# Optimization experiments

Hardware: AMD Instinct MI355X
Metric: run time of the kernel (lower is better)

## Reference

```python
import jax, jax.numpy as jnp
import numpy as np
import math

N_NODES, N_EDGES, NNZ, D, L = 100000, 20000, 500000, 128, 4
ALPHA, LAMDA = 0.1, 0.5


def setup_inputs() -> dict:
    key = jax.random.key(0)
    ks = jax.random.split(key, 16)
    x = jax.random.normal(ks[0], (N_NODES, D), jnp.float32)
    e = jax.random.normal(ks[1], (N_EDGES, D), jnp.float32)
    nodes = jax.random.randint(ks[2], (NNZ,), 0, N_NODES)
    edges = jnp.sort(jax.random.randint(ks[3], (NNZ,), 0, N_EDGES)).at[-1].set(N_EDGES - 1)
    hyperedge_index = jnp.stack([nodes, edges]).astype(jnp.int32)
    dist_v2e = jax.random.randint(ks[4], (NNZ,), 0, 64).astype(jnp.float32)
    deg_v2e = jax.random.randint(ks[5], (NNZ,), 0, 64).astype(jnp.float32)
    dist_e2v = jax.random.randint(ks[6], (NNZ,), 0, 64).astype(jnp.float32)
    deg_e2v = jax.random.randint(ks[7], (NNZ,), 0, 64).astype(jnp.float32)
    s = 0.05
    W0 = jax.random.normal(ks[8], (D, D), jnp.float32) * s
    b0 = jnp.zeros((D,), jnp.float32)
    Wn = jax.random.normal(ks[9], (L, D, D), jnp.float32) * s
    We = jax.random.normal(ks[10], (L, D, D), jnp.float32) * s
    attn_w = jax.random.normal(ks[11], (L, 2 * D), jnp.float32) * s
    attn_b = jnp.zeros((L,), jnp.float32)
    wd_w = jax.random.normal(ks[12], (L,), jnp.float32) * s
    wd_b = jnp.zeros((L,), jnp.float32)
    wg_w = jax.random.normal(ks[13], (L,), jnp.float32) * s
    wg_b = jnp.zeros((L,), jnp.float32)
    return dict(x=x, e=e, hyperedge_index=hyperedge_index, dist_v2e=dist_v2e,
                deg_v2e=deg_v2e, dist_e2v=dist_e2v, deg_e2v=deg_e2v,
                W0=W0, b0=b0, Wn=Wn, We=We, attn_w=attn_w, attn_b=attn_b,
                wd_w=wd_w, wd_b=wd_b, wg_w=wg_w, wg_b=wg_b)


def _seg_softmax(s, idx, num):
    # numerically-stable scatter_softmax over segments idx
    m = jax.ops.segment_max(s, idx, num_segments=num)
    ex = jnp.exp(s - m[idx])
    den = jax.ops.segment_sum(ex, idx, num_segments=num)
    return ex / den[idx]


def _forward(x, e, hei, dv2e, gv2e, de2v, ge2v, W0, b0, Wn, We, aw, ab, wdw, wdb, wgw, wgb):
    nodes, edges = hei[0], hei[1]
    N, E = x.shape[0], e.shape[0]
    ones = jnp.ones(nodes.shape[0], x.dtype)
    dV = jax.ops.segment_sum(ones, nodes, num_segments=N)
    cnt = jax.ops.segment_sum(ones, edges, num_segments=E)
    dE = jax.ops.segment_sum(dV[nodes], edges, num_segments=E) / jnp.maximum(cnt, 1.0)
    degV = jnp.where(dV > 0, dV ** -0.5, 1.0)[:, None]   # [N,1]
    degE = jnp.where(dE > 0, dE ** -0.5, 1.0)[:, None]   # [E,1]

    x = jax.nn.relu(x @ W0 + b0)
    x0, e0 = x, e
    d = x.shape[1]
    for i in range(L):
        beta = math.log(LAMDA / (i + 1) + 1.0)
        # v2e attention: concat [x[nodes], e[edges]] -> softmax over edge segments
        sx1 = x @ aw[i, :d]; se1 = e @ aw[i, d:]
        s_v2e = sx1[nodes] + se1[edges] + ab[i] + dv2e * wdw[i] + wdb[i] + gv2e * wgw[i] + wgb[i]
        a_v2e = _seg_softmax(s_v2e, edges, E)[:, None]
        # e2v attention (flipped): concat [e[edges], x[nodes]] -> softmax over node segments
        se2 = e @ aw[i, :d]; sx2 = x @ aw[i, d:]
        s_e2v = se2[edges] + sx2[nodes] + ab[i] + de2v * wdw[i] + wdb[i] + ge2v * wgw[i] + wgb[i]
        a_e2v = _seg_softmax(s_e2v, nodes, N)[:, None]

        Xe1 = jax.ops.segment_sum(x[nodes] * a_v2e, edges, num_segments=E) * degE
        Xv1 = jax.ops.segment_sum(Xe1[edges] * a_e2v, nodes, num_segments=N) * degV
        Xv2 = jax.ops.segment_sum(e[edges] * a_e2v, nodes, num_segments=N) * degV
        Xe2 = jax.ops.segment_sum(Xv2[nodes] * a_v2e, edges, num_segments=E) * degE
        xm = (Xv1 + Xv2) * 0.5
        em = (Xe1 + Xe2) * 0.5
        xi = (1 - ALPHA) * xm + ALPHA * x0
        x = (1 - beta) * xi + beta * (xi @ Wn[i])
        ei = (1 - ALPHA) * em + ALPHA * e0
        e = (1 - beta) * ei + beta * (ei @ We[i])
        if i < L - 1:
            x = jax.nn.relu(x)
            e = jax.nn.relu(e)
    return x, e


def reference(x, e, hyperedge_index, dist_v2e, deg_v2e, dist_e2v, deg_e2v,
              W0, b0, Wn, We, attn_w, attn_b, wd_w, wd_b, wg_w, wg_b):
    return _forward(x, e, hyperedge_index, dist_v2e, deg_v2e, dist_e2v, deg_e2v,
                    W0, b0, Wn, We, attn_w, attn_b, wd_w, wd_b, wg_w, wg_b)
```

## Files before the change

### kernel.cpp

```cpp
#include <hip/hip_runtime.h>
#include <hip/hip_fp16.h>
#include <math.h>

#define DD 128
#define SCAN_BLOCKS 256
#define SMAX_CAP 128

typedef _Float16 f16x8 __attribute__((ext_vector_type(8)));
typedef float f32x4 __attribute__((ext_vector_type(4)));

__device__ inline float wave_sum(float v){
#pragma unroll
  for (int m = 32; m >= 1; m >>= 1) v += __shfl_xor(v, m, 64);
  return v;
}
__device__ inline int wave_sum_i(int v){
#pragma unroll
  for (int m = 32; m >= 1; m >>= 1) v += __shfl_xor(v, m, 64);
  return v;
}


__global__ void k_edge_offsets(const int* __restrict__ edges, int nnz, int E,
                               int* __restrict__ eo){
  int e = blockIdx.x * blockDim.x + threadIdx.x;
  if (e > E) return;
  int lo = 0, hi = nnz;
  while (lo < hi){ int mid = (lo + hi) >> 1; if (edges[mid] < e) lo = mid + 1; else hi = mid; }
  eo[e] = lo;
}

__global__ void k_hist(const int* __restrict__ nodes, int nnz, int* __restrict__ dV){
  int k = blockIdx.x * blockDim.x + threadIdx.x;
  if (k < nnz) atomicAdd(&dV[nodes[k]], 1);
}

__global__ __launch_bounds__(256) void k_scan_partial(const int* __restrict__ dV, int N,
                                                      int* __restrict__ part){
  int b = blockIdx.x, t = threadIdx.x;
  int chunk = (N + SCAN_BLOCKS - 1) / SCAN_BLOCKS;
  int s0 = b * chunk, s1 = min(s0 + chunk, N);
  int sum = 0;
  for (int n = s0 + t; n < s1; n += 256) sum += dV[n];
  sum = wave_sum_i(sum);
  __shared__ int wred[4];
  int lane = t & 63, wid = t >> 6;
  if (lane == 0) wred[wid] = sum;
  __syncthreads();
  if (t == 0) part[b] = wred[0] + wred[1] + wred[2] + wred[3];
}

__global__ __launch_bounds__(SCAN_BLOCKS) void k_scan_blocksums(int* __restrict__ part){
  __shared__ int sh[SCAN_BLOCKS];
  int t = threadIdx.x;
  int v = part[t];
  sh[t] = v; __syncthreads();
  for (int off = 1; off < SCAN_BLOCKS; off <<= 1){
    int add = (t >= off) ? sh[t - off] : 0;
    __syncthreads();
    sh[t] += add;
    __syncthreads();
  }
  part[t] = sh[t] - v;
}

__global__ __launch_bounds__(256) void k_scan_apply(const int* __restrict__ dV, int N, int nnz,
    const int* __restrict__ partScan, int* __restrict__ no, int* __restrict__ nfill,
    float* __restrict__ degV){
  int b = blockIdx.x, t = threadIdx.x;
  int chunk = (N + SCAN_BLOCKS - 1) / SCAN_BLOCKS;
  int s0 = b * chunk, s1 = min(s0 + chunk, N);
  int lane = t & 63, wid = t >> 6;
  __shared__ int wtot[4];
  __shared__ int s_run;
  if (t == 0) s_run = partScan[b];
  __syncthreads();
  for (int base = s0; base < s1; base += 256){
    int n = base + t;
    int d = (n < s1) ? dV[n] : 0;
    int v = d;
#pragma unroll
    for (int off = 1; off < 64; off <<= 1){
      int o = __shfl_up(v, off, 64);
      if (lane >= off) v += o;
    }
    if (lane == 63) wtot[wid] = v;
    __syncthreads();
    int run0 = s_run;
    int woff = 0;
    for (int w = 0; w < wid; w++) woff += wtot[w];
    if (n < s1){
      int excl = run0 + woff + v - d;
      no[n] = excl; nfill[n] = excl;
      degV[n] = d > 0 ? 1.0f / sqrtf((float)d) : 1.0f;
    }
    int btot = wtot[0] + wtot[1] + wtot[2] + wtot[3];
    __syncthreads();
    if (t == 0) s_run = run0 + btot;
    __syncthreads();
  }
  if (b == 0 && t == 0) no[N] = nnz;
}

__global__ void k_permpack(const int* __restrict__ nodes, const int* __restrict__ edges,
                           const float* __restrict__ dist, const float* __restrict__ deg,
                           int nnz, int* __restrict__ nfill, float2* __restrict__ pack){
  int k = blockIdx.x * blockDim.x + threadIdx.x;
  if (k < nnz){
    int pos = atomicAdd(&nfill[nodes[k]], 1);
    pack[pos] = make_float2(__int_as_float(edges[k]), dist[k] + 64.f * deg[k]);
  }
}

__global__ void k_edge_deg(const int* __restrict__ nodes, const int* __restrict__ eo, int E,
                           const int* __restrict__ dV, float* __restrict__ degE){
  int e = blockIdx.x * blockDim.x + threadIdx.x;
  if (e >= E) return;
  int b = eo[e], en = eo[e + 1];
  float s = 0.f;
  for (int k = b; k < en; k++) s += (float)dV[nodes[k]];
  float cnt = (float)(en - b);
  float dE = s / fmaxf(cnt, 1.0f);
  degE[e] = dE > 0.f ? 1.0f / sqrtf(dE) : 1.0f;
}

__global__ __launch_bounds__(256) void k_einit(const float2* __restrict__ e_in2,
    const float* __restrict__ aw1, const float* __restrict__ aw2,
    int E, __half2* __restrict__ e0h,
    float* __restrict__ se1, float* __restrict__ se2){
  int wave = threadIdx.x >> 6, lane = threadIdx.x & 63;
  int e = blockIdx.x * 4 + wave;
  if (e >= E) return;
  float2 v = e_in2[(size_t)e * 64 + lane];
  e0h[(size_t)e * 64 + lane] = __floats2half2_rn(v.x, v.y);
  float2 a2v = ((const float2*)aw2)[lane];
  float2 a1v = ((const float2*)aw1)[lane];
  float s1 = v.x * a2v.x + v.y * a2v.y;
  float s2 = v.x * a1v.x + v.y * a1v.y;
  s1 = wave_sum(s1); s2 = wave_sum(s2);
  if (lane == 0){ se1[e] = s1; se2[e] = s2; }
}

__global__ void k_wcast(const float* __restrict__ W0, const float* __restrict__ Wn,
                        const float* __restrict__ We, _Float16* __restrict__ Wt){
  int idx = blockIdx.x * 256 + threadIdx.x;
  if (idx >= 9 * 16384) return;
  int m = idx >> 14, r = idx & 16383;
  int n = r >> 7, k = r & 127;
  float v;
  if (m == 0){
    v = W0[k * 128 + n];
  } else {
    int i = (m <= 4) ? m - 1 : m - 5;
    const float* src = (m <= 4) ? Wn + (size_t)i * 16384 : We + (size_t)i * 16384;
    float beta = logf(0.5f / (float)(i + 1) + 1.0f);
    v = beta * src[k * 128 + n] + ((n == k) ? (1.0f - beta) : 0.f);
  }
  Wt[(size_t)m * 16384 + n * 128 + k] = (_Float16)v;
}


__device__ inline void acc8h(const float4 q, float w, float* a){
  float2 h0 = __half22float2(*(const __half2*)&q.x);
  float2 h1 = __half22float2(*(const __half2*)&q.y);
  float2 h2v = __half22float2(*(const __half2*)&q.z);
  float2 h3 = __half22float2(*(const __half2*)&q.w);
  a[0] += w * h0.x; a[1] += w * h0.y; a[2] += w * h1.x; a[3] += w * h1.y;
  a[4] += w * h2v.x; a[5] += w * h2v.y; a[6] += w * h3.x; a[7] += w * h3.y;
}

__global__ __launch_bounds__(256) void k_sma1(
    const int* __restrict__ nodes, const int* __restrict__ eo,
    const float* __restrict__ sx1, const float* __restrict__ se1,
    const float* __restrict__ dist, const float* __restrict__ deg,
    const float* __restrict__ ab, const float* __restrict__ wdw, const float* __restrict__ wdb,
    const float* __restrict__ wgw, const float* __restrict__ wgb, int li,
    const float* __restrict__ degE, const float4* __restrict__ xh4,
    const _Float16* __restrict__ ehL,
    int E, float* __restrict__ a_v2e, float* __restrict__ esc, _Float16* __restrict__ ETraw){
  __shared__ float lw[8][SMAX_CAP];
  int l32 = threadIdx.x & 31;
  int grp = threadIdx.x >> 5;
  int e = blockIdx.x * 8 + grp;
  if (e >= E) return;
  int b = eo[e], en = eo[e + 1];
  int l16 = l32 & 15, hf = l32 >> 4;
  if (b >= en){
    if (l32 == 0) esc[e] = 0.f;
    if (hf == 0){
      f16x8 ehv = *(const f16x8*)(ehL + (size_t)e * 128 + 8 * l16);
      f16x8 o0, o1;
#pragma unroll
      for (int q = 0; q < 2; q++){
        o0[4 * q] = (_Float16)0.f; o0[4 * q + 1] = (_Float16)0.f;
        o0[4 * q + 2] = ehv[2 * q]; o0[4 * q + 3] = ehv[2 * q + 1];
        o1[4 * q] = (_Float16)0.f; o1[4 * q + 1] = (_Float16)0.f;
        o1[4 * q + 2] = ehv[2 * q + 4]; o1[4 * q + 3] = ehv[2 * q + 5];
      }
      _Float16* dst = ETraw + (size_t)e * 256 + 16 * l16;
      *(f16x8*)dst = o0; *(f16x8*)(dst + 8) = o1;
    }
    return;
  }
  float base = se1[e] + ab[li] + wdb[li] + wgb[li];
  float wd = wdw[li], wg = wgw[li];
  float m = -INFINITY;
  float sreg[4];
#pragma unroll
  for (int c = 0; c < 4; c++){
    int k = b + l32 + 32 * c;
    if (k < en){
      float s = sx1[nodes[k]] + base + dist[k] * wd + deg[k] * wg;
      sreg[c] = s; m = fmaxf(m, s);
    }
  }
  for (int k = b + l32 + SMAX_CAP; k < en; k += 32){
    float s = sx1[nodes[k]] + base + dist[k] * wd + deg[k] * wg;
    m = fmaxf(m, s);
  }
#pragma unroll
  for (int mm = 16; mm >= 1; mm >>= 1) m = fmaxf(m, __shfl_xor(m, mm, 32));
  float sum = 0.f;
#pragma unroll
  for (int c = 0; c < 4; c++){
    int k = b + l32 + 32 * c;
    if (k < en){
      float ex = __expf(sreg[c] - m);
      a_v2e[k] = ex; lw[grp][l32 + 32 * c] = ex; sum += ex;
    }
  }
  for (int k = b + l32 + SMAX_CAP; k < en; k += 32){
    float s = sx1[nodes[k]] + base + dist[k] * wd + deg[k] * wg;
    float ex = __expf(s - m);
    a_v2e[k] = ex; sum += ex;
  }
#pragma unroll
  for (int mm = 16; mm >= 1; mm >>= 1) sum += __shfl_xor(sum, mm, 32);
  float sc = degE[e] / sum;
  if (l32 == 0) esc[e] = sc;
  float a[8] = {0.f, 0.f, 0.f, 0.f, 0.f, 0.f, 0.f, 0.f};
  int k = b + hf;
  for (; k + 2 < en; k += 4){
    int n0 = nodes[k], n1 = nodes[k + 2];
    float w0 = (k - b < SMAX_CAP) ? lw[grp][k - b] : a_v2e[k];
    float w1 = (k + 2 - b < SMAX_CAP) ? lw[grp][k + 2 - b] : a_v2e[k + 2];
    float4 v0 = xh4[(size_t)n0 * 16 + l16];
    float4 v1 = xh4[(size_t)n1 * 16 + l16];
    acc8h(v0, w0, a); acc8h(v1, w1, a);
  }
  for (; k < en; k += 2){
    int n = nodes[k];
    float w = (k - b < SMAX_CAP) ? lw[grp][k - b] : a_v2e[k];
    float4 v = xh4[(size_t)n * 16 + l16];
    acc8h(v, w, a);
  }
#pragma unroll
  for (int j = 0; j < 8; j++) a[j] += __shfl_xor(a[j], 16, 32);
  if (hf == 0){
    f16x8 ehv = *(const f16x8*)(ehL + (size_t)e * 128 + 8 * l16);
    f16x8 o0, o1;
#pragma unroll
    for (int q = 0; q < 2; q++){
      __half2 xa = __floats2half2_rn(a[2 * q] * sc, a[2 * q + 1] * sc);
      o0[4 * q] = ((_Float16*)&xa)[0]; o0[4 * q + 1] = ((_Float16*)&xa)[1];
      o0[4 * q + 2] = ehv[2 * q]; o0[4 * q + 3] = ehv[2 * q + 1];
      __half2 xb = __floats2half2_rn(a[2 * q + 4] * sc, a[2 * q + 5] * sc);
      o1[4 * q] = ((_Float16*)&xb)[0]; o1[4 * q + 1] = ((_Float16*)&xb)[1];
      o1[4 * q + 2] = ehv[2 * q + 4]; o1[4 * q + 3] = ehv[2 * q + 5];
    }
    _Float16* dst = ETraw + (size_t)e * 256 + 16 * l16;
    *(f16x8*)dst = o0; *(f16x8*)(dst + 8) = o1;
  }
}

__device__ inline void acc8(const float4 q, float w, float* a1, float* a2){
  float2 x0 = __half22float2(*(const __half2*)&q.x);
  float2 e0 = __half22float2(*(const __half2*)&q.y);
  float2 x1 = __half22float2(*(const __half2*)&q.z);
  float2 e1 = __half22float2(*(const __half2*)&q.w);
  a1[0] += w * x0.x; a1[1] += w * x0.y; a1[2] += w * x1.x; a1[3] += w * x1.y;
  a2[0] += w * e0.x; a2[1] += w * e0.y; a2[2] += w * e1.x; a2[3] += w * e1.y;
}

__global__ __launch_bounds__(256) void k_agg2f(
    const float2* __restrict__ pack, const int* __restrict__ no,
    const float* __restrict__ se2, const float* __restrict__ sx2,
    const float* __restrict__ ab, const float* __restrict__ wdw, const float* __restrict__ wdb,
    const float* __restrict__ wgw, const float* __restrict__ wgb, int li,
    const float4* __restrict__ ETq,
    const float* __restrict__ degV, const __half2* __restrict__ x0h,
    int N, __half2* __restrict__ Xv2h, __half2* __restrict__ xiH){
  int l32 = threadIdx.x & 31;
  int grp = threadIdx.x >> 5;
  int n = blockIdx.x * 8 + grp;
  if (n >= N) return;
  int b = no[n], en = no[n + 1];
  float base = sx2[n] + ab[li] + wdb[li] + wgb[li];
  float wd = wdw[li], wg = wgw[li];
  float2 x0v2 = *(const float2*)&x0h[(size_t)n * 64 + 2 * l32];
  float l_run = 0.f;
  float a1[4] = {0.f, 0.f, 0.f, 0.f}, a2[4] = {0.f, 0.f, 0.f, 0.f};
  if (en - b <= 32){
    int cs = en - b;
    float s = -INFINITY; int e_l = 0;
    if (l32 < cs){
      float2 pk = pack[b + l32];
      e_l = __float_as_int(pk.x);
      int vi = (int)pk.y;
      s = se2[e_l] + base + (float)(vi & 63) * wd + (float)(vi >> 6) * wg;
    }
    float m_c = s;
#pragma unroll
    for (int mm = 16; mm >= 1; mm >>= 1) m_c = fmaxf(m_c, __shfl_xor(m_c, mm, 32));
    float p = (l32 < cs) ? __expf(s - m_c) : 0.f;
    l_run = p;
#pragma unroll
    for (int mm = 16; mm >= 1; mm >>= 1) l_run += __shfl_xor(l_run, mm, 32);
    int jj = 0;
    for (; jj + 7 < cs; jj += 8){
      float w[8]; int ei[8]; float4 q[8];
#pragma unroll
      for (int u = 0; u < 8; u++){
        w[u] = __shfl(p, jj + u, 32);
        ei[u] = __shfl(e_l, jj + u, 32);
      }
#pragma unroll
      for (int u = 0; u < 8; u++) q[u] = ETq[(size_t)ei[u] * 32 + l32];
#pragma unroll
      for (int u = 0; u < 8; u++) acc8(q[u], w[u], a1, a2);
    }
    for (; jj + 3 < cs; jj += 4){
      float w[4]; int ei[4]; float4 q[4];
#pragma unroll
      for (int u = 0; u < 4; u++){
        w[u] = __shfl(p, jj + u, 32);
        ei[u] = __shfl(e_l, jj + u, 32);
      }
#pragma unroll
      for (int u = 0; u < 4; u++) q[u] = ETq[(size_t)ei[u] * 32 + l32];
#pragma unroll
      for (int u = 0; u < 4; u++) acc8(q[u], w[u], a1, a2);
    }
    for (; jj < cs; jj++){
      float w = __shfl(p, jj, 32);
      int ei_ = __shfl(e_l, jj, 32);
      float4 q = ETq[(size_t)ei_ * 32 + l32];
      acc8(q, w, a1, a2);
    }
  } else {
    float m_run = -INFINITY;
    for (int cb = b; cb < en; cb += 32){
      int cs = min(32, en - cb);
      float s = -INFINITY; int e_l = 0;
      if (l32 < cs){
        float2 pk = pack[cb + l32];
        e_l = __float_as_int(pk.x);
        int vi = (int)pk.y;
        s = se2[e_l] + base + (float)(vi & 63) * wd + (float)(vi >> 6) * wg;
      }
      float m_c = s;
#pragma unroll
      for (int mm = 16; mm >= 1; mm >>= 1) m_c = fmaxf(m_c, __shfl_xor(m_c, mm, 32));
      float p = (l32 < cs) ? __expf(s - m_c) : 0.f;
      float l_c = p;
#pragma unroll
      for (int mm = 16; mm >= 1; mm >>= 1) l_c += __shfl_xor(l_c, mm, 32);
      float m_new = fmaxf(m_run, m_c);
      float f_old = __expf(m_run - m_new);
      float f_c = __expf(m_c - m_new);
#pragma unroll
      for (int r = 0; r < 4; r++){ a1[r] *= f_old; a2[r] *= f_old; }
      l_run = l_run * f_old + l_c * f_c;
      m_run = m_new;
      int jj = 0;
      for (; jj + 3 < cs; jj += 4){
        float w0 = __shfl(p, jj, 32) * f_c;
        float w1 = __shfl(p, jj + 1, 32) * f_c;
        float w2 = __shfl(p, jj + 2, 32) * f_c;
        float w3 = __shfl(p, jj + 3, 32) * f_c;
        int e0i = __shfl(e_l, jj, 32);
        int e1i = __shfl(e_l, jj + 1, 32);
        int e2i = __shfl(e_l, jj + 2, 32);
        int e3i = __shfl(e_l, jj + 3, 32);
        float4 q0 = ETq[(size_t)e0i * 32 + l32];
        float4 q1 = ETq[(size_t)e1i * 32 + l32];
        float4 q2 = ETq[(size_t)e2i * 32 + l32];
        float4 q3 = ETq[(size_t)e3i * 32 + l32];
        acc8(q0, w0, a1, a2);
        acc8(q1, w1, a1, a2);
        acc8(q2, w2, a1, a2);
        acc8(q3, w3, a1, a2);
      }
      for (; jj < cs; jj++){
        float w = __shfl(p, jj, 32) * f_c;
        int ei_ = __shfl(e_l, jj, 32);
        float4 q = ETq[(size_t)ei_ * 32 + l32];
        acc8(q, w, a1, a2);
      }
    }
  }
  float inv = l_run > 0.f ? 1.0f / l_run : 0.f;
  float dv = degV[n] * inv;
  float2 st;
  *(__half2*)&st.x = __floats2half2_rn(a2[0] * dv, a2[1] * dv);
  *(__half2*)&st.y = __floats2half2_rn(a2[2] * dv, a2[3] * dv);
  *(float2*)&Xv2h[(size_t)n * 64 + 2 * l32] = st;
  float2 h0 = __half22float2(*(const __half2*)&x0v2.x);
  float2 h1 = __half22float2(*(const __half2*)&x0v2.y);
  float2 xo;
  *(__half2*)&xo.x = __floats2half2_rn(0.45f * dv * (a1[0] + a2[0]) + 0.1f * h0.x,
                                       0.45f * dv * (a1[1] + a2[1]) + 0.1f * h0.y);
  *(__half2*)&xo.y = __floats2half2_rn(0.45f * dv * (a1[2] + a2[2]) + 0.1f * h1.x,
                                       0.45f * dv * (a1[3] + a2[3]) + 0.1f * h1.y);
  *(float2*)&xiH[(size_t)n * 64 + 2 * l32] = xo;
}

__global__ __launch_bounds__(256) void k_agg3(const int* __restrict__ nodes, const int* __restrict__ eo,
    const float4* __restrict__ Xv2h4, const float* __restrict__ a_v2e, const float* __restrict__ esc,
    const float4* __restrict__ ETq, const float4* __restrict__ e0h4,
    int E, __half2* __restrict__ eiH){
  int l32 = threadIdx.x & 31;
  int grp = threadIdx.x >> 5;
  int e = blockIdx.x * 8 + grp;
  if (e >= E) return;
  int b = eo[e], en = eo[e + 1];
  int l16 = l32 & 15, hf = l32 >> 4;
  float a[8] = {0.f, 0.f, 0.f, 0.f, 0.f, 0.f, 0.f, 0.f};
  int k = b + hf;
  for (; k + 2 < en; k += 4){
    int n0 = nodes[k], n1 = nodes[k + 2];
    float w0 = a_v2e[k], w1 = a_v2e[k + 2];
    float4 v0 = Xv2h4[(size_t)n0 * 16 + l16];
    float4 v1 = Xv2h4[(size_t)n1 * 16 + l16];
    acc8h(v0, w0, a); acc8h(v1, w1, a);
  }
  for (; k < en; k += 2){
    int n = nodes[k];
    float w = a_v2e[k];
    float4 v = Xv2h4[(size_t)n * 16 + l16];
    acc8h(v, w, a);
  }
#pragma unroll
  for (int j = 0; j < 8; j++) a[j] += __shfl_xor(a[j], 16, 32);
  if (hf == 0){
    float dE = esc[e];
    float4 q0 = ETq[(size_t)e * 32 + 2 * l16];
    float4 q1 = ETq[(size_t)e * 32 + 2 * l16 + 1];
    float2 x01 = __half22float2(*(const __half2*)&q0.x);
    float2 x23 = __half22float2(*(const __half2*)&q0.z);
    float2 x45 = __half22float2(*(const __half2*)&q1.x);
    float2 x67 = __half22float2(*(const __half2*)&q1.z);
    float4 ev = e0h4[(size_t)e * 16 + l16];
    float2 g0 = __half22float2(*(const __half2*)&ev.x);
    float2 g1 = __half22float2(*(const __half2*)&ev.y);
    float2 g2 = __half22float2(*(const __half2*)&ev.z);
    float2 g3 = __half22float2(*(const __half2*)&ev.w);
    float4 o;
    *(__half2*)&o.x = __floats2half2_rn(0.45f * (x01.x + a[0] * dE) + 0.1f * g0.x,
                                        0.45f * (x01.y + a[1] * dE) + 0.1f * g0.y);
    *(__half2*)&o.y = __floats2half2_rn(0.45f * (x23.x + a[2] * dE) + 0.1f * g1.x,
                                        0.45f * (x23.y + a[3] * dE) + 0.1f * g1.y);
    *(__half2*)&o.z = __floats2half2_rn(0.45f * (x45.x + a[4] * dE) + 0.1f * g2.x,
                                        0.45f * (x45.y + a[5] * dE) + 0.1f * g2.y);
    *(__half2*)&o.w = __floats2half2_rn(0.45f * (x67.x + a[6] * dE) + 0.1f * g3.x,
                                        0.45f * (x67.y + a[7] * dE) + 0.1f * g3.y);
    *(float4*)&eiH[(size_t)e * 64 + 4 * l16] = o;
  }
}

__device__ __forceinline__ void gemm_body(
    const _Float16* __restrict__ Ah, const _Float16* __restrict__ Wt,
    float* __restrict__ outf, _Float16* __restrict__ outh,
    const float* __restrict__ awA, const float* __restrict__ awB,
    float* __restrict__ sA, float* __restrict__ sB,
    int nrows, int do_relu, int blockRow0, _Float16 (*sh)[136]){
  int lane = threadIdx.x & 63, wave = threadIdx.x >> 6;
  int row0 = blockRow0 + wave * 16;
  int lm = lane & 15;
  int lk8 = (lane >> 4) * 8;
  int rbase = (lane >> 4) * 4;
  if (row0 < nrows){
    int arow = row0 + lm; if (arow >= nrows) arow = nrows - 1;
    f16x8 afrag[4];
#pragma unroll
    for (int ks = 0; ks < 4; ks++)
      afrag[ks] = *(const f16x8*)(Ah + (size_t)arow * 128 + ks * 32 + lk8);
    float da[4] = {0.f, 0.f, 0.f, 0.f}, db[4] = {0.f, 0.f, 0.f, 0.f};
    for (int t = 0; t < 8; t++){
      f32x4 acc = {0.f, 0.f, 0.f, 0.f};
#pragma unroll
      for (int ks = 0; ks < 4; ks++){
        f16x8 bf = *(const f16x8*)(Wt + (size_t)(t * 16 + lm) * 128 + ks * 32 + lk8);
        acc = __builtin_amdgcn_mfma_f32_16x16x32_f16(afrag[ks], bf, acc, 0, 0, 0);
      }
      int col = t * 16 + lm;
      float wa = 0.f, wb = 0.f;
      if (awA){ wa = awA[col]; wb = awB[col]; }
#pragma unroll
      for (int r = 0; r < 4; r++){
        int gr = row0 + rbase + r;
        float v = acc[r];
        if (do_relu) v = fmaxf(v, 0.f);
        if (outf && gr < nrows) outf[(size_t)gr * 128 + col] = v;
        if (outh) sh[wave * 16 + rbase + r][col] = (_Float16)v;
        if (gr < nrows){ da[r] += v * wa; db[r] += v * wb; }
      }
    }
    if (awA){
#pragma unroll
      for (int r = 0; r < 4; r++){
        float a = da[r], bb = db[r];
#pragma unroll
        for (int m = 8; m >= 1; m >>= 1){
          a += __shfl_xor(a, m, 64);
          bb += __shfl_xor(bb, m, 64);
        }
        int gr = row0 + rbase + r;
        if (lm == 0 && gr < nrows){ sA[gr] = a; sB[gr] = bb; }
      }
    }
  }
  if (outh){
    __syncthreads();
    for (int i = threadIdx.x; i < 64 * 16; i += 256){
      int rr = i >> 4, cc = (i & 15) * 8;
      int gr = blockRow0 + rr;
      if (gr < nrows)
        *(f16x8*)(outh + (size_t)gr * 128 + cc) = *(const f16x8*)&sh[rr][cc];
    }
  }
}

__global__ __launch_bounds__(256) void k_gemm2(
    const _Float16* __restrict__ Ax, const _Float16* __restrict__ Wx,
    const _Float16* __restrict__ Ae, const _Float16* __restrict__ Wte,
    float* __restrict__ outfx, _Float16* __restrict__ outhx,
    float* __restrict__ outfe, _Float16* __restrict__ outhe,
    const float* __restrict__ awAx, const float* __restrict__ awBx,
    float* __restrict__ sAx, float* __restrict__ sBx,
    const float* __restrict__ awAe, const float* __restrict__ awBe,
    float* __restrict__ sAe, float* __restrict__ sBe,
    int nrx, int nre, int nbx, int do_relu){
  __shared__ _Float16 sh[64][136];
  if ((int)blockIdx.x < nbx){
    gemm_body(Ax, Wx, outfx, outhx, awAx, awBx, sAx, sBx, nrx, do_relu,
              blockIdx.x * 64, sh);
  } else {
    gemm_body(Ae, Wte, outfe, outhe, awAe, awBe, sAe, sBe, nre, do_relu,
              (blockIdx.x - nbx) * 64, sh);
  }
}

__global__ __launch_bounds__(256) void k_gemm0(
    const float* __restrict__ Af, const _Float16* __restrict__ Wt,
    const float* __restrict__ bias,
    _Float16* __restrict__ outh, _Float16* __restrict__ outh2,
    const float* __restrict__ awA, const float* __restrict__ awB,
    float* __restrict__ sA, float* __restrict__ sB, int nrows){
  __shared__ _Float16 sh[64][136];
  int wave = threadIdx.x >> 6, lane = threadIdx.x & 63;
  int blockRow0 = blockIdx.x * 64;
  int row0 = blockRow0 + wave * 16;
  int lm = lane & 15;
  int lk8 = (lane >> 4) * 8;
  int rbase = (lane >> 4) * 4;
  if (row0 < nrows){
    int arow = row0 + lm; if (arow >= nrows) arow = nrows - 1;
    const float* ap = Af + (size_t)arow * 128;
    f16x8 afrag[4];
#pragma unroll
    for (int ks = 0; ks < 4; ks++){
      float4 v0 = *(const float4*)(ap + ks * 32 + lk8);
      float4 v1 = *(const float4*)(ap + ks * 32 + lk8 + 4);
      f16x8 a;
      a[0] = (_Float16)v0.x; a[1] = (_Float16)v0.y; a[2] = (_Float16)v0.z; a[3] = (_Float16)v0.w;
      a[4] = (_Float16)v1.x; a[5] = (_Float16)v1.y; a[6] = (_Float16)v1.z; a[7] = (_Float16)v1.w;
      afrag[ks] = a;
    }
    float da[4] = {0.f, 0.f, 0.f, 0.f}, db[4] = {0.f, 0.f, 0.f, 0.f};
    for (int t = 0; t < 8; t++){
      f32x4 acc = {0.f, 0.f, 0.f, 0.f};
#pragma unroll
      for (int ks = 0; ks < 4; ks++){
        f16x8 bf = *(const f16x8*)(Wt + (size_t)(t * 16 + lm) * 128 + ks * 32 + lk8);
        acc = __builtin_amdgcn_mfma_f32_16x16x32_f16(afrag[ks], bf, acc, 0, 0, 0);
      }
      int col = t * 16 + lm;
      float wa = awA[col], wb = awB[col];
      float bi = bias[col];
#pragma unroll
      for (int r = 0; r < 4; r++){
        int gr = row0 + rbase + r;
        float v = fmaxf(acc[r] + bi, 0.f);
        sh[wave * 16 + rbase + r][col] = (_Float16)v;
        if (gr < nrows){ da[r] += v * wa; db[r] += v * wb; }
      }
    }
#pragma unroll
    for (int r = 0; r < 4; r++){
      float a = da[r], bb = db[r];
#pragma unroll
      for (int m = 8; m >= 1; m >>= 1){
        a += __shfl_xor(a, m, 64);
        bb += __shfl_xor(bb, m, 64);
      }
      int gr = row0 + rbase + r;
      if (lm == 0 && gr < nrows){ sA[gr] = a; sB[gr] = bb; }
    }
  }
  __syncthreads();
  for (int i = threadIdx.x; i < 64 * 16; i += 256){
    int rr = i >> 4, cc = (i & 15) * 8;
    int gr = blockRow0 + rr;
    if (gr < nrows){
      f16x8 v = *(const f16x8*)&sh[rr][cc];
      *(f16x8*)(outh + (size_t)gr * 128 + cc) = v;
      *(f16x8*)(outh2 + (size_t)gr * 128 + cc) = v;
    }
  }
}


extern "C" void kernel_launch(void* const* d_in, const int* in_sizes, int n_in,
                              void* d_out, int out_size, void* d_ws, size_t ws_size,
                              hipStream_t stream) {
  const float* x_in     = (const float*)d_in[0];
  const float* e_in     = (const float*)d_in[1];
  const int*   hei      = (const int*)d_in[2];
  const float* dist_v2e = (const float*)d_in[3];
  const float* deg_v2e  = (const float*)d_in[4];
  const float* dist_e2v = (const float*)d_in[5];
  const float* deg_e2v  = (const float*)d_in[6];
  const float* W0       = (const float*)d_in[7];
  const float* b0       = (const float*)d_in[8];
  const float* Wn       = (const float*)d_in[9];
  const float* We       = (const float*)d_in[10];
  const float* attn_w   = (const float*)d_in[11];
  const float* attn_b   = (const float*)d_in[12];
  const float* wd_w     = (const float*)d_in[13];
  const float* wd_b     = (const float*)d_in[14];
  const float* wg_w     = (const float*)d_in[15];
  const float* wg_b     = (const float*)d_in[16];

  const int N   = in_sizes[0] / DD;
  const int E   = in_sizes[1] / DD;
  const int NNZ = in_sizes[2] / 2;
  const int* nodesArr = hei;
  const int* edgesArr = hei + NNZ;

  float* out_x = (float*)d_out;
  float* out_e = (float*)d_out + (size_t)N * DD;

  __half2* xh   = (__half2*)((char*)out_x + (size_t)N * DD * 2);
  _Float16* ETraw = (_Float16*)out_e;
  const float4* ETq = (const float4*)out_e;

  char* wsp = (char*)d_ws;
  auto alloc = [&](size_t bytes) -> void* {
    void* p = (void*)wsp;
    wsp += (bytes + 255) / 256 * 256;
    return p;
  };
  _Float16* x0h  = (_Float16*)alloc((size_t)N * DD * 2);
  _Float16* Xv2h = (_Float16*)alloc((size_t)N * DD * 2);
  _Float16* xiH  = (_Float16*)alloc((size_t)N * DD * 2);
  _Float16* eiH  = (_Float16*)alloc((size_t)E * DD * 2);
  _Float16* e0h  = (_Float16*)alloc((size_t)E * DD * 2);
  _Float16* ehL  = (_Float16*)alloc((size_t)E * DD * 2);
  _Float16* Wt   = (_Float16*)alloc((size_t)9 * 16384 * 2);
  float* sx1   = (float*)alloc((size_t)N * 4);
  float* sx2   = (float*)alloc((size_t)N * 4);
  float* se1   = (float*)alloc((size_t)E * 4);
  float* se2   = (float*)alloc((size_t)E * 4);
  float* a_v2e = (float*)alloc((size_t)NNZ * 4);
  float* degV  = (float*)alloc((size_t)N * 4);
  float* degE  = (float*)alloc((size_t)E * 4);
  float* esc   = (float*)alloc((size_t)E * 4);
  float2* pack = (float2*)alloc((size_t)NNZ * 8);
  int* dV_i  = (int*)alloc((size_t)N * 4);
  int* no_   = (int*)alloc((size_t)(N + 1) * 4);
  int* nfill = (int*)alloc((size_t)N * 4);
  int* eo    = (int*)alloc((size_t)(E + 1) * 4);
  int* part  = (int*)alloc((size_t)SCAN_BLOCKS * 4);

  hipMemsetAsync(dV_i, 0, (size_t)N * 4, stream);
  k_edge_offsets<<<(E + 1 + 255) / 256, 256, 0, stream>>>(edgesArr, NNZ, E, eo);
  k_hist<<<(NNZ + 255) / 256, 256, 0, stream>>>(nodesArr, NNZ, dV_i);
  k_scan_partial<<<SCAN_BLOCKS, 256, 0, stream>>>(dV_i, N, part);
  k_scan_blocksums<<<1, SCAN_BLOCKS, 0, stream>>>(part);
  k_scan_apply<<<SCAN_BLOCKS, 256, 0, stream>>>(dV_i, N, NNZ, part, no_, nfill, degV);
  k_permpack<<<(NNZ + 255) / 256, 256, 0, stream>>>(nodesArr, edgesArr, dist_e2v, deg_e2v,
                                                    NNZ, nfill, pack);
  k_edge_deg<<<(E + 255) / 256, 256, 0, stream>>>(nodesArr, eo, E, dV_i, degE);
  k_wcast<<<(9 * 16384 + 255) / 256, 256, 0, stream>>>(W0, Wn, We, Wt);

  const float* aw1_0 = attn_w;
  const float* aw2_0 = attn_w + 128;

  k_einit<<<(E + 3) / 4, 256, 0, stream>>>((const float2*)e_in, aw1_0, aw2_0,
                                            E, (__half2*)e0h, se1, se2);

  k_gemm0<<<(N + 63) / 64, 256, 0, stream>>>(x_in, Wt, b0,
      (_Float16*)xh, x0h, aw1_0, aw2_0, sx1, sx2, N);

  const int nbx = (N + 63) / 64, nbe = (E + 63) / 64;
  for (int i = 0; i < 4; i++){
    const float* aw1n = (i < 3) ? attn_w + (size_t)(i + 1) * 256        : nullptr;
    const float* aw2n = (i < 3) ? attn_w + (size_t)(i + 1) * 256 + 128  : nullptr;
    const _Float16* ehCur = (i == 0) ? e0h : ehL;

    k_sma1<<<(E + 7) / 8, 256, 0, stream>>>(nodesArr, eo, sx1, se1,
        dist_v2e, deg_v2e, attn_b, wd_w, wd_b, wg_w, wg_b, i, degE,
        (const float4*)xh, ehCur, E, a_v2e, esc, ETraw);

    k_agg2f<<<(N + 7) / 8, 256, 0, stream>>>(pack, no_, se2, sx2,
        attn_b, wd_w, wd_b, wg_w, wg_b, i,
        ETq, degV, (const __half2*)x0h, N, (__half2*)Xv2h, (__half2*)xiH);

    k_agg3<<<(E + 7) / 8, 256, 0, stream>>>(nodesArr, eo, (const float4*)Xv2h,
        a_v2e, esc, ETq, (const float4*)e0h, E, (__half2*)eiH);

    k_gemm2<<<nbx + nbe, 256, 0, stream>>>(
        xiH, Wt + (size_t)(1 + i) * 16384,
        eiH, Wt + (size_t)(5 + i) * 16384,
        (i == 3) ? out_x : nullptr, (i < 3) ? (_Float16*)xh : nullptr,
        (i == 3) ? out_e : nullptr, (i < 3) ? ehL : nullptr,
        aw1n, aw2n, sx1, sx2,
        aw2n, aw1n, se1, se2,
        N, E, nbx, i < 3 ? 1 : 0);
  }
}
```

Before: 825.7 us.

## Assign one full 64-lane wavefront per segment in aggregation kernels

The three segment-aggregation kernels (v2e softmax+gather, e2v aggregation, v2e second pass) now give each edge or node a whole 64-lane wave instead of a 32-lane half-wave. The extra lanes process more neighbours in parallel and are combined with additional cross-lane shuffles before the write. The aim is more memory-level parallelism per segment, which helps the longer edge segments (about 25 entries on average). The cost is twice as many blocks, extra reductions, and idle lanes on short node segments (about 5 entries on average), which may waste wave slots in k_agg2f.

```diff
diff --git a/kernel.cpp b/kernel.cpp
--- a/kernel.cpp
+++ b/kernel.cpp
@@ -178,16 +178,16 @@
     const float* __restrict__ degE, const float4* __restrict__ xh4,
     const _Float16* __restrict__ ehL,
     int E, float* __restrict__ a_v2e, float* __restrict__ esc, _Float16* __restrict__ ETraw){
-  __shared__ float lw[8][SMAX_CAP];
-  int l32 = threadIdx.x & 31;
-  int grp = threadIdx.x >> 5;
-  int e = blockIdx.x * 8 + grp;
+  __shared__ float lw[4][SMAX_CAP];
+  int lane = threadIdx.x & 63;
+  int wave = threadIdx.x >> 6;
+  int e = blockIdx.x * 4 + wave;
   if (e >= E) return;
   int b = eo[e], en = eo[e + 1];
-  int l16 = l32 & 15, hf = l32 >> 4;
+  int l16 = lane & 15, q16 = lane >> 4;
   if (b >= en){
-    if (l32 == 0) esc[e] = 0.f;
-    if (hf == 0){
+    if (lane == 0) esc[e] = 0.f;
+    if (q16 == 0){
       f16x8 ehv = *(const f16x8*)(ehL + (size_t)e * 128 + 8 * l16);
       f16x8 o0, o1;
 #pragma unroll
@@ -205,58 +205,61 @@
   float base = se1[e] + ab[li] + wdb[li] + wgb[li];
   float wd = wdw[li], wg = wgw[li];
   float m = -INFINITY;
-  float sreg[4];
-#pragma unroll
-  for (int c = 0; c < 4; c++){
-    int k = b + l32 + 32 * c;
+  float sreg[2];
+#pragma unroll
+  for (int c = 0; c < 2; c++){
+    int k = b + lane + 64 * c;
     if (k < en){
       float s = sx1[nodes[k]] + base + dist[k] * wd + deg[k] * wg;
       sreg[c] = s; m = fmaxf(m, s);
     }
   }
-  for (int k = b + l32 + SMAX_CAP; k < en; k += 32){
+  for (int k = b + lane + SMAX_CAP; k < en; k += 64){
     float s = sx1[nodes[k]] + base + dist[k] * wd + deg[k] * wg;
     m = fmaxf(m, s);
   }
 #pragma unroll
-  for (int mm = 16; mm >= 1; mm >>= 1) m = fmaxf(m, __shfl_xor(m, mm, 32));
+  for (int mm = 32; mm >= 1; mm >>= 1) m = fmaxf(m, __shfl_xor(m, mm, 64));
   float sum = 0.f;
 #pragma unroll
-  for (int c = 0; c < 4; c++){
-    int k = b + l32 + 32 * c;
+  for (int c = 0; c < 2; c++){
+    int k = b + lane + 64 * c;
     if (k < en){
       float ex = __expf(sreg[c] - m);
-      a_v2e[k] = ex; lw[grp][l32 + 32 * c] = ex; sum += ex;
-    }
-  }
-  for (int k = b + l32 + SMAX_CAP; k < en; k += 32){
+      a_v2e[k] = ex; lw[wave][lane + 64 * c] = ex; sum += ex;
+    }
+  }
+  for (int k = b + lane + SMAX_CAP; k < en; k += 64){
     float s = sx1[nodes[k]] + base + dist[k] * wd + deg[k] * wg;
     float ex = __expf(s - m);
     a_v2e[k] = ex; sum += ex;
   }
 #pragma unroll
-  for (int mm = 16; mm >= 1; mm >>= 1) sum += __shfl_xor(sum, mm, 32);
+  for (int mm = 32; mm >= 1; mm >>= 1) sum += __shfl_xor(sum, mm, 64);
   float sc = degE[e] / sum;
-  if (l32 == 0) esc[e] = sc;
+  if (lane == 0) esc[e] = sc;
   float a[8] = {0.f, 0.f, 0.f, 0.f, 0.f, 0.f, 0.f, 0.f};
-  int k = b + hf;
-  for (; k + 2 < en; k += 4){
-    int n0 = nodes[k], n1 = nodes[k + 2];
-    float w0 = (k - b < SMAX_CAP) ? lw[grp][k - b] : a_v2e[k];
-    float w1 = (k + 2 - b < SMAX_CAP) ? lw[grp][k + 2 - b] : a_v2e[k + 2];
+  int k = b + q16;
+  for (; k + 4 < en; k += 8){
+    float w0 = (k - b < SMAX_CAP) ? lw[wave][k - b] : a_v2e[k];
+    float w1 = (k + 4 - b < SMAX_CAP) ? lw[wave][k + 4 - b] : a_v2e[k + 4];
+    int n0 = nodes[k], n1 = nodes[k + 4];
     float4 v0 = xh4[(size_t)n0 * 16 + l16];
     float4 v1 = xh4[(size_t)n1 * 16 + l16];
     acc8h(v0, w0, a); acc8h(v1, w1, a);
   }
-  for (; k < en; k += 2){
+  for (; k < en; k += 4){
+    float w = (k - b < SMAX_CAP) ? lw[wave][k - b] : a_v2e[k];
     int n = nodes[k];
-    float w = (k - b < SMAX_CAP) ? lw[grp][k - b] : a_v2e[k];
     float4 v = xh4[(size_t)n * 16 + l16];
     acc8h(v, w, a);
   }
 #pragma unroll
-  for (int j = 0; j < 8; j++) a[j] += __shfl_xor(a[j], 16, 32);
-  if (hf == 0){
+  for (int j = 0; j < 8; j++){
+    a[j] += __shfl_xor(a[j], 16, 64);
+    a[j] += __shfl_xor(a[j], 32, 64);
+  }
+  if (q16 == 0){
     f16x8 ehv = *(const f16x8*)(ehL + (size_t)e * 128 + 8 * l16);
     f16x8 o0, o1;
 #pragma unroll
@@ -290,9 +293,10 @@
     const float4* __restrict__ ETq,
     const float* __restrict__ degV, const __half2* __restrict__ x0h,
     int N, __half2* __restrict__ Xv2h, __half2* __restrict__ xiH){
-  int l32 = threadIdx.x & 31;
-  int grp = threadIdx.x >> 5;
-  int n = blockIdx.x * 8 + grp;
+  int lane = threadIdx.x & 63;
+  int wave = threadIdx.x >> 6;
+  int l32 = lane & 31, half = lane >> 5;
+  int n = blockIdx.x * 4 + wave;
   if (n >= N) return;
   int b = no[n], en = no[n + 1];
   float base = sx2[n] + ab[li] + wdb[li] + wgb[li];
@@ -317,34 +321,22 @@
 #pragma unroll
     for (int mm = 16; mm >= 1; mm >>= 1) l_run += __shfl_xor(l_run, mm, 32);
     int jj = 0;
-    for (; jj + 7 < cs; jj += 8){
-      float w[8]; int ei[8]; float4 q[8];
-#pragma unroll
-      for (int u = 0; u < 8; u++){
-        w[u] = __shfl(p, jj + u, 32);
-        ei[u] = __shfl(e_l, jj + u, 32);
-      }
-#pragma unroll
-      for (int u = 0; u < 8; u++) q[u] = ETq[(size_t)ei[u] * 32 + l32];
-#pragma unroll
-      for (int u = 0; u < 8; u++) acc8(q[u], w[u], a1, a2);
-    }
     for (; jj + 3 < cs; jj += 4){
-      float w[4]; int ei[4]; float4 q[4];
-#pragma unroll
-      for (int u = 0; u < 4; u++){
-        w[u] = __shfl(p, jj + u, 32);
-        ei[u] = __shfl(e_l, jj + u, 32);
-      }
-#pragma unroll
-      for (int u = 0; u < 4; u++) q[u] = ETq[(size_t)ei[u] * 32 + l32];
-#pragma unroll
-      for (int u = 0; u < 4; u++) acc8(q[u], w[u], a1, a2);
-    }
-    for (; jj < cs; jj++){
-      float w = __shfl(p, jj, 32);
-      int ei_ = __shfl(e_l, jj, 32);
-      float4 q = ETq[(size_t)ei_ * 32 + l32];
+      int i0 = jj + half, i1 = jj + 2 + half;
+      float w0 = __shfl(p, i0, 32), w1 = __shfl(p, i1, 32);
+      int e0i = __shfl(e_l, i0, 32), e1i = __shfl(e_l, i1, 32);
+      float4 q0 = ETq[(size_t)e0i * 32 + l32];
+      float4 q1 = ETq[(size_t)e1i * 32 + l32];
+      acc8(q0, w0, a1, a2);
+      acc8(q1, w1, a1, a2);
+    }
+    for (; jj < cs; jj += 2){
+      int idx = jj + half;
+      int idxc = min(idx, cs - 1);
+      float wr = __shfl(p, idxc, 32);
+      int er = __shfl(e_l, idxc, 32);
+      float w = (idx < cs) ? wr : 0.f;
+      float4 q = ETq[(size_t)er * 32 + l32];
       acc8(q, w, a1, a2);
     }
   } else {
@@ -374,75 +366,79 @@
       m_run = m_new;
       int jj = 0;
       for (; jj + 3 < cs; jj += 4){
-        float w0 = __shfl(p, jj, 32) * f_c;
-        float w1 = __shfl(p, jj + 1, 32) * f_c;
-        float w2 = __shfl(p, jj + 2, 32) * f_c;
-        float w3 = __shfl(p, jj + 3, 32) * f_c;
-        int e0i = __shfl(e_l, jj, 32);
-        int e1i = __shfl(e_l, jj + 1, 32);
-        int e2i = __shfl(e_l, jj + 2, 32);
-        int e3i = __shfl(e_l, jj + 3, 32);
+        int i0 = jj + half, i1 = jj + 2 + half;
+        float w0 = __shfl(p, i0, 32) * f_c, w1 = __shfl(p, i1, 32) * f_c;
+        int e0i = __shfl(e_l, i0, 32), e1i = __shfl(e_l, i1, 32);
         float4 q0 = ETq[(size_t)e0i * 32 + l32];
         float4 q1 = ETq[(size_t)e1i * 32 + l32];
-        float4 q2 = ETq[(size_t)e2i * 32 + l32];
-        float4 q3 = ETq[(size_t)e3i * 32 + l32];
         acc8(q0, w0, a1, a2);
         acc8(q1, w1, a1, a2);
-        acc8(q2, w2, a1, a2);
-        acc8(q3, w3, a1, a2);
-      }
-      for (; jj < cs; jj++){
-        float w = __shfl(p, jj, 32) * f_c;
-        int ei_ = __shfl(e_l, jj, 32);
-        float4 q = ETq[(size_t)ei_ * 32 + l32];
+      }
+      for (; jj < cs; jj += 2){
+        int idx = jj + half;
+        int idxc = min(idx, cs - 1);
+        float wr = __shfl(p, idxc, 32);
+        int er = __shfl(e_l, idxc, 32);
+        float w = (idx < cs) ? wr * f_c : 0.f;
+        float4 q = ETq[(size_t)er * 32 + l32];
         acc8(q, w, a1, a2);
       }
     }
   }
-  float inv = l_run > 0.f ? 1.0f / l_run : 0.f;
-  float dv = degV[n] * inv;
-  float2 st;
-  *(__half2*)&st.x = __floats2half2_rn(a2[0] * dv, a2[1] * dv);
-  *(__half2*)&st.y = __floats2half2_rn(a2[2] * dv, a2[3] * dv);
-  *(float2*)&Xv2h[(size_t)n * 64 + 2 * l32] = st;
-  float2 h0 = __half22float2(*(const __half2*)&x0v2.x);
-  float2 h1 = __half22float2(*(const __half2*)&x0v2.y);
-  float2 xo;
-  *(__half2*)&xo.x = __floats2half2_rn(0.45f * dv * (a1[0] + a2[0]) + 0.1f * h0.x,
-                                       0.45f * dv * (a1[1] + a2[1]) + 0.1f * h0.y);
-  *(__half2*)&xo.y = __floats2half2_rn(0.45f * dv * (a1[2] + a2[2]) + 0.1f * h1.x,
-                                       0.45f * dv * (a1[3] + a2[3]) + 0.1f * h1.y);
-  *(float2*)&xiH[(size_t)n * 64 + 2 * l32] = xo;
+#pragma unroll
+  for (int r = 0; r < 4; r++){
+    a1[r] += __shfl_xor(a1[r], 32, 64);
+    a2[r] += __shfl_xor(a2[r], 32, 64);
+  }
+  if (half == 0){
+    float inv = l_run > 0.f ? 1.0f / l_run : 0.f;
+    float dv = degV[n] * inv;
+    float2 st;
+    *(__half2*)&st.x = __floats2half2_rn(a2[0] * dv, a2[1] * dv);
+    *(__half2*)&st.y = __floats2half2_rn(a2[2] * dv, a2[3] * dv);
+    *(float2*)&Xv2h[(size_t)n * 64 + 2 * l32] = st;
+    float2 h0 = __half22float2(*(const __half2*)&x0v2.x);
+    float2 h1 = __half22float2(*(const __half2*)&x0v2.y);
+    float2 xo;
+    *(__half2*)&xo.x = __floats2half2_rn(0.45f * dv * (a1[0] + a2[0]) + 0.1f * h0.x,
+                                         0.45f * dv * (a1[1] + a2[1]) + 0.1f * h0.y);
+    *(__half2*)&xo.y = __floats2half2_rn(0.45f * dv * (a1[2] + a2[2]) + 0.1f * h1.x,
+                                         0.45f * dv * (a1[3] + a2[3]) + 0.1f * h1.y);
+    *(float2*)&xiH[(size_t)n * 64 + 2 * l32] = xo;
+  }
 }
 
 __global__ __launch_bounds__(256) void k_agg3(const int* __restrict__ nodes, const int* __restrict__ eo,
     const float4* __restrict__ Xv2h4, const float* __restrict__ a_v2e, const float* __restrict__ esc,
     const float4* __restrict__ ETq, const float4* __restrict__ e0h4,
     int E, __half2* __restrict__ eiH){
-  int l32 = threadIdx.x & 31;
-  int grp = threadIdx.x >> 5;
-  int e = blockIdx.x * 8 + grp;
+  int lane = threadIdx.x & 63;
+  int wave = threadIdx.x >> 6;
+  int e = blockIdx.x * 4 + wave;
   if (e >= E) return;
   int b = eo[e], en = eo[e + 1];
-  int l16 = l32 & 15, hf = l32 >> 4;
+  int l16 = lane & 15, q16 = lane >> 4;
   float a[8] = {0.f, 0.f, 0.f, 0.f, 0.f, 0.f, 0.f, 0.f};
-  int k = b + hf;
-  for (; k + 2 < en; k += 4){
-    int n0 = nodes[k], n1 = nodes[k + 2];
-    float w0 = a_v2e[k], w1 = a_v2e[k + 2];
+  int k = b + q16;
+  for (; k + 4 < en; k += 8){
+    float w0 = a_v2e[k], w1 = a_v2e[k + 4];
+    int n0 = nodes[k], n1 = nodes[k + 4];
     float4 v0 = Xv2h4[(size_t)n0 * 16 + l16];
     float4 v1 = Xv2h4[(size_t)n1 * 16 + l16];
     acc8h(v0, w0, a); acc8h(v1, w1, a);
   }
-  for (; k < en; k += 2){
+  for (; k < en; k += 4){
+    float w = a_v2e[k];
     int n = nodes[k];
-    float w = a_v2e[k];
     float4 v = Xv2h4[(size_t)n * 16 + l16];
     acc8h(v, w, a);
   }
 #pragma unroll
-  for (int j = 0; j < 8; j++) a[j] += __shfl_xor(a[j], 16, 32);
-  if (hf == 0){
+  for (int j = 0; j < 8; j++){
+    a[j] += __shfl_xor(a[j], 16, 64);
+    a[j] += __shfl_xor(a[j], 32, 64);
+  }
+  if (q16 == 0){
     float dE = esc[e];
     float4 q0 = ETq[(size_t)e * 32 + 2 * l16];
     float4 q1 = ETq[(size_t)e * 32 + 2 * l16 + 1];
@@ -709,15 +705,15 @@
     const float* aw2n = (i < 3) ? attn_w + (size_t)(i + 1) * 256 + 128  : nullptr;
     const _Float16* ehCur = (i == 0) ? e0h : ehL;
 
-    k_sma1<<<(E + 7) / 8, 256, 0, stream>>>(nodesArr, eo, sx1, se1,
+    k_sma1<<<(E + 3) / 4, 256, 0, stream>>>(nodesArr, eo, sx1, se1,
         dist_v2e, deg_v2e, attn_b, wd_w, wd_b, wg_w, wg_b, i, degE,
         (const float4*)xh, ehCur, E, a_v2e, esc, ETraw);
 
-    k_agg2f<<<(N + 7) / 8, 256, 0, stream>>>(pack, no_, se2, sx2,
+    k_agg2f<<<(N + 3) / 4, 256, 0, stream>>>(pack, no_, se2, sx2,
         attn_b, wd_w, wd_b, wg_w, wg_b, i,
         ETq, degV, (const __half2*)x0h, N, (__half2*)Xv2h, (__half2*)xiH);
 
-    k_agg3<<<(E + 7) / 8, 256, 0, stream>>>(nodesArr, eo, (const float4*)Xv2h,
+    k_agg3<<<(E + 3) / 4, 256, 0, stream>>>(nodesArr, eo, (const float4*)Xv2h,
         a_v2e, esc, ETq, (const float4*)e0h, E, (__half2*)eiH);
 
     k_gemm2<<<nbx + nbe, 256, 0, stream>>>(
```

Measured after the change: 821.5 us. About the same (-0.5%).
